# Kernel tuning notes

Hardware: AMD Instinct MI355X
Metric: run time of the kernel (lower is better)

Reference implementation:

```python
import jax, jax.numpy as jnp
import numpy as np

B, T, V, S = 32, 2048, 1024, 256
BLANK = 0
NEG = -1e30  # log-space 'zero' (avoids inf so zero_infinity handling is a simple threshold)


def setup_inputs() -> dict:
    key = jax.random.key(0)
    k1, k2, k3, k4 = jax.random.split(key, 4)
    # valid log-probabilities, as produced by an upstream log_softmax head
    preds_logprob = jax.nn.log_softmax(
        jax.random.normal(k1, (B, T, V), dtype=jnp.float32), axis=-1)
    tokens_gt = jax.random.randint(k2, (B, S), 1, V)            # labels exclude blank=0
    cqt_lens = jax.random.randint(k3, (B,), T // 2, T + 1)      # input lengths
    token_lens_gt = jax.random.randint(k4, (B,), S // 2, S + 1) # target lengths (>=1)
    return {"preds_logprob": preds_logprob, "tokens_gt": tokens_gt,
            "cqt_lens": cqt_lens, "token_lens_gt": token_lens_gt}


def _ctc_single(lp, ext, rep_ok, Tl, Sl):
    """Negative CTC log-likelihood for one sample.
    lp: [T, V] log-probs; ext: [L=2S+1] extended label seq (blanks interleaved);
    rep_ok: [L] bool, whether the s-2 -> s skip transition is allowed;
    Tl: input length; Sl: target length (>=1)."""
    emit = lp[:, ext]  # [T, L] emission log-probs, gathered once outside the scan
    L = ext.shape[0]
    alpha = jnp.full((L,), NEG, dtype=lp.dtype)
    alpha = alpha.at[0].set(emit[0, 0]).at[1].set(emit[0, 1])

    neg1 = jnp.full((1,), NEG, dtype=lp.dtype)
    neg2 = jnp.full((2,), NEG, dtype=lp.dtype)

    def step(alpha, xs):
        e, t = xs
        a1 = jnp.concatenate([neg1, alpha[:-1]])
        a2 = jnp.concatenate([neg2, alpha[:-2]])
        a2 = jnp.where(rep_ok, a2, NEG)
        m = jnp.maximum(jnp.maximum(alpha, a1), a2)
        new = e + m + jnp.log(jnp.exp(alpha - m) + jnp.exp(a1 - m) + jnp.exp(a2 - m))
        # freeze the lattice past this sample's input length (masking by cqt_lens)
        alpha = jnp.where(t < Tl, new, alpha)
        return alpha, None

    ts = jnp.arange(1, lp.shape[0])
    alpha, _ = jax.lax.scan(step, alpha, (emit[1:], ts))

    # log-likelihood = logsumexp over the two terminal lattice states
    lA = alpha[2 * Sl]
    lB = alpha[2 * Sl - 1]
    m = jnp.maximum(lA, lB)
    ll = m + jnp.log(jnp.exp(lA - m) + jnp.exp(lB - m))
    return -ll


def _ctc_loss(preds_logprob, tokens_gt, cqt_lens, token_lens_gt):
    # mask_by_length: zero out frames past cqt_lens (no effect on CTC value,
    # kept for faithfulness); swapaxes(0,1) is a pure layout change.
    tmask = jnp.arange(T)[None, :] < cqt_lens[:, None]          # [B, T]
    lp = preds_logprob * tmask[:, :, None].astype(preds_logprob.dtype)

    # extended label sequence with blanks interleaved: [blank, y1, blank, ..., yS, blank]
    ext = jnp.zeros((B, 2 * S + 1), dtype=tokens_gt.dtype).at[:, 1::2].set(tokens_gt)
    ext_m2 = jnp.concatenate([jnp.zeros((B, 2), dtype=ext.dtype), ext[:, :-2]], axis=1)
    rep_ok = (ext != BLANK) & (ext != ext_m2)                   # allow s-2 skip

    losses = jax.vmap(_ctc_single)(lp, ext, rep_ok, cqt_lens, token_lens_gt)  # [B]
    # zero_infinity=True: unreachable alignments produce ~ -NEG; zero them out
    losses = jnp.where(losses > 1e29, 0.0, losses)
    # reduction='mean': divide by target length, then mean over batch
    return jnp.mean(losses / token_lens_gt.astype(losses.dtype))


def reference(preds_logprob, tokens_gt, cqt_lens, token_lens_gt):
    return _ctc_loss(preds_logprob, tokens_gt, cqt_lens, token_lens_gt)
```

## Files before the change

kernel.cpp:

```cpp
#include <hip/hip_runtime.h>
#include <math.h>

#define BB 32
#define TT 2048
#define VV 1024
#define SS 256
#define TCHUNK 4
#define CH 16
#define NSLOT 3

__device__ __forceinline__ void async_ld16(const float* g, const float* l) {
    __builtin_amdgcn_global_load_lds(
        (const __attribute__((address_space(1))) void*)(uintptr_t)g,
        (__attribute__((address_space(3))) void*)(unsigned)(uintptr_t)l, 16, 0, 0);
}
__device__ __forceinline__ void async_ld4(const float* g, const float* l) {
    __builtin_amdgcn_global_load_lds(
        (const __attribute__((address_space(1))) void*)(uintptr_t)g,
        (__attribute__((address_space(3))) void*)(unsigned)(uintptr_t)l, 4, 0, 0);
}
#define WAIT_VM0() __builtin_amdgcn_s_waitcnt(0x0F70)

__device__ __forceinline__ float dpp_shr1_f(float x) {
    int r = __builtin_amdgcn_update_dpp(0, __float_as_int(x), 0x138, 0xF, 0xF, true);
    return __int_as_float(r);
}
__device__ __forceinline__ int dpp_shr1_i(int x) {
    return __builtin_amdgcn_update_dpp(0, x, 0x138, 0xF, 0xF, true);
}
__device__ __forceinline__ float max3f(float a, float b, float c) {
    float d;
    asm("v_max3_f32 %0, %1, %2, %3" : "=v"(d) : "v"(a), "v"(b), "v"(c));
    return d;
}

__global__ __launch_bounds__(256) void ctc_pre(const float* __restrict__ lp,
    const int* __restrict__ tokens, const int* __restrict__ cqt,
    const int* __restrict__ slen, float* __restrict__ G, float* __restrict__ Gbl,
    float* __restrict__ out)
{
    __shared__ __align__(16) float rows[TCHUNK][VV];
    __shared__ int toks[SS];
    const int tid = threadIdx.x;
    const int bx  = blockIdx.x;
    if (bx == 0 && tid == 0) out[0] = 0.f;
    const int nchunk = TT / TCHUNK;
    const int b  = bx / nchunk;
    const int t0 = (bx % nchunk) * TCHUNK;
    const int Tl = cqt[b];
    if (t0 >= Tl) return;
    const int Sl = slen[b];
    toks[tid] = tokens[b * SS + tid];
#pragma unroll
    for (int k = 0; k < TCHUNK; ++k) {
        const int t = t0 + k;
        if (t < Tl)
            ((float4*)rows[k])[tid] = ((const float4*)(lp + ((size_t)b * TT + t) * VV))[tid];
    }
    __syncthreads();
#pragma unroll
    for (int k = 0; k < TCHUNK; ++k) {
        const int t = t0 + k;
        if (t >= Tl) break;
        const float pb0 = rows[k][0];
        float* gp = G + ((size_t)b * TT + t) * 256;
        gp[tid] = (tid < Sl) ? __expf(rows[k][toks[tid]] - pb0) : 0.f;
        if (tid == 0) Gbl[b * TT + t] = pb0;
    }
}

__global__ __launch_bounds__(256) void ctc_walk(const float* __restrict__ G,
    const float* __restrict__ Gbl, const int* __restrict__ tokens,
    const int* __restrict__ cqt, const int* __restrict__ slen, float* __restrict__ out)
{
    __shared__ __align__(16) float tokL[NSLOT][CH * 256];
    __shared__ __align__(16) float blkL[NSLOT][64];
    __shared__ float als[513];
    __shared__ int   aE[65];
    __shared__ int   ready[NSLOT];
    __shared__ int   prog;

    const int b    = blockIdx.x;
    const int tid  = threadIdx.x;
    const int wid  = tid >> 6;
    const int lane = tid & 63;
    const int Tl   = cqt[b];
    const float* __restrict__ Gb   = G   + (size_t)b * TT * 256;
    const float* __restrict__ GblB = Gbl + (size_t)b * TT;

    if (tid < NSLOT) ready[tid] = -1;
    if (tid == NSLOT) prog = -1;
    __syncthreads();

    const int NC = (Tl + 14) >> 4;
    volatile int* vready = ready;
    volatile int* vprog  = &prog;

    if (wid != 0) {
        const int slot = wid - 1;
        for (int c = wid - 1; c < NC; c += 3) {
            while (*vprog < c - NSLOT) {}
            __builtin_amdgcn_sched_barrier(0);
            asm volatile("" ::: "memory");
            const int tbase = 1 + (c << 4);
            const float* lt = tokL[slot];
#pragma unroll
            for (int k = 0; k < CH; ++k) {
                int tt = tbase + k; tt = (tt < Tl) ? tt : (Tl - 1);
                async_ld16(Gb + (size_t)tt * 256 + (lane << 2), lt + k * 256);
            }
            int tbk = tbase + lane; tbk = (tbk < Tl) ? tbk : (Tl - 1);
            async_ld4(GblB + tbk, blkL[slot]);
            WAIT_VM0();
            __builtin_amdgcn_sched_barrier(0);
            asm volatile("" ::: "memory");
            vready[slot] = c;
        }
        return;
    }

    const int Sl = slen[b];
    const int j0 = lane * 4;
    const int* tb = tokens + b * SS;
    const int tm1 = (j0 == 0) ? 0 : tb[j0 - 1];
    const int q0 = tb[j0], q1 = tb[j0 + 1], q2 = tb[j0 + 2], q3 = tb[j0 + 3];
    const float m0 = (q0 != tm1) ? 1.f : 0.f;
    const float m1 = (q1 != q0)  ? 1.f : 0.f;
    const float m2 = (q2 != q1)  ? 1.f : 0.f;
    const float m3 = (q3 != q2)  ? 1.f : 0.f;
    const float lzm = (lane == 0) ? 0.f : 1.f;

    float a0=0.f,a1=0.f,a2=0.f,a3=0.f,a4=0.f,a5=0.f,a6=0.f,a7=0.f,aX=0.f;
    if (lane == 0) {
        const float e0 = __expf(GblB[0]);
        a0 = e0;
        a1 = Gb[0] * e0;
    }
    int    Etot = 0;
    float  sfac = lzm;
    double bacc = 0.0;

#define LOADCHUNK(s) do { \
    _Pragma("unroll") \
    for (int k = 0; k < CH; ++k) { \
        pr[k] = ((const float4*)(tokL[s] + (k << 8)))[lane]; \
        pb[k] = blkL[s][k]; \
    } \
} while (0)

#define ONESTEP(P4) do { \
    const float h1 = dpp_shr1_f(a7) * sfac; \
    const float n0 = a0 + h1; \
    const float n1 = (P4).x * (a1 + a0 + m0 * h1); \
    const float n2 = a2 + a1; \
    const float n3 = (P4).y * (a3 + a2 + m1 * a1); \
    const float n4 = a4 + a3; \
    const float n5 = (P4).z * (a5 + a4 + m2 * a3); \
    const float n6 = a6 + a5; \
    const float n7 = (P4).w * (a7 + a6 + m3 * a5); \
    aX = aX + a7; \
    a0=n0;a1=n1;a2=n2;a3=n3;a4=n4;a5=n5;a6=n6;a7=n7; \
} while (0)

#define RENORM_LOCAL() do { \
    const float mm = max3f(max3f(a0,a1,a2), max3f(a3,a4,a5), max3f(a6,a7,aX)); \
    int ee = (__float_as_int(mm) >> 23) - 126; \
    ee = (mm > 0.f) ? ee : 0; \
    const float sc = __int_as_float((127 - ee) << 23); \
    a0*=sc;a1*=sc;a2*=sc;a3*=sc;a4*=sc;a5*=sc;a6*=sc;a7*=sc;aX*=sc; \
    Etot += ee; \
    int Ep = dpp_shr1_i(Etot); \
    if (mm == 0.f && lane > 0) Etot = Ep; \
    Ep = dpp_shr1_i(Etot); \
    if (mm == 0.f && lane > 0) Etot = Ep; \
    int dd = Ep - Etot; \
    dd = (dd < -126) ? -126 : ((dd > 100) ? 100 : dd); \
    sfac = __int_as_float((127 + dd) << 23) * lzm; \
} while (0)

    float4 pr[CH];
    float  pb[CH];

    const int F = (Tl - 1) >> 4;
    int slot = 0;
    for (int c = 0; c < NC; ++c) {
        while (vready[slot] < c) {}
        __builtin_amdgcn_sched_barrier(0);
        asm volatile("" ::: "memory");
        LOADCHUNK(slot);
        asm volatile("" ::: "memory");
        *vprog = c;
        if (c < F) {
            float bt = ((pb[0]+pb[1])+(pb[2]+pb[3]))+((pb[4]+pb[5])+(pb[6]+pb[7]));
            bt += ((pb[8]+pb[9])+(pb[10]+pb[11]))+((pb[12]+pb[13])+(pb[14]+pb[15]));
            bacc += (double)bt;
#pragma unroll
            for (int k = 0; k < CH; ++k) {
                ONESTEP(pr[k]);
                if ((k & 3) == 3) RENORM_LOCAL();
            }
        } else {
            const int nv = (Tl - 1) - (F << 4);
            float bt = 0.f;
#pragma unroll
            for (int k = 0; k < CH; ++k) {
                if (k < nv) { bt += pb[k]; ONESTEP(pr[k]); }
                if ((k & 3) == 3) RENORM_LOCAL();
            }
            bacc += (double)bt;
        }
        slot = (slot == NSLOT - 1) ? 0 : slot + 1;
    }

    als[8 * lane + 0] = a0; als[8 * lane + 1] = a1;
    als[8 * lane + 2] = a2; als[8 * lane + 3] = a3;
    als[8 * lane + 4] = a4; als[8 * lane + 5] = a5;
    als[8 * lane + 6] = a6; als[8 * lane + 7] = a7;
    aE[lane] = Etot;
    if (lane == 63) { als[512] = aX; aE[64] = Etot; }
    asm volatile("s_waitcnt lgkmcnt(0)" ::: "memory");
    if (lane == 0) {
        const int sA = 2 * Sl, sB = 2 * Sl - 1;
        const float vA = als[sA], vB = als[sB];
        const int   eA = aE[sA >> 3], eB = aE[sB >> 3];
        int em;
        if (vA > 0.f && vB > 0.f) em = (eA > eB) ? eA : eB;
        else if (vA > 0.f)        em = eA;
        else if (vB > 0.f)        em = eB;
        else                      em = 0;
        const double s = ldexp((double)vA, eA - em) + ldexp((double)vB, eB - em);
        double loss = -(log(s) + (double)em * 0.6931471805599453 + bacc);
        if (!(loss < 1e29)) loss = 0.0;
        atomicAdd(out, (float)(loss / ((double)Sl * (double)BB)));
    }
#undef LOADCHUNK
#undef ONESTEP
#undef RENORM_LOCAL
}

extern "C" void kernel_launch(void* const* d_in, const int* in_sizes, int n_in,
                              void* d_out, int out_size, void* d_ws, size_t ws_size,
                              hipStream_t stream)
{
    const float* lp     = (const float*)d_in[0];
    const int*   tokens = (const int*)d_in[1];
    const int*   cqt    = (const int*)d_in[2];
    const int*   slen   = (const int*)d_in[3];
    float* out = (float*)d_out;
    float* G   = (float*)d_ws;
    float* Gbl = G + (size_t)BB * TT * 256;

    hipLaunchKernelGGL(ctc_pre,  dim3(BB * (TT / TCHUNK)), dim3(256), 0, stream,
                       lp, tokens, cqt, slen, G, Gbl, out);
    hipLaunchKernelGGL(ctc_walk, dim3(BB), dim3(256), 0, stream,
                       G, Gbl, tokens, cqt, slen, out);
}
```

Baseline: 486.0 us.

## Split CTC lattice walk across two wavefronts in a wavefront pipeline

The serial alpha recursion, previously run by a single wavefront owning 8 lattice states per lane, is split so wave 0 handles the first half of the lattice and wave 1 the second half. Each lane now owns 4 states. Wave 0 publishes its boundary value and exponents per chunk through double-buffered shared memory, and wave 1 consumes them one chunk behind. This halves per-step arithmetic on the critical path at the cost of cross-wave spin synchronisation, extra shared-memory traffic and one more wave per block (320 threads).

```diff
diff --git a/kernel.cpp b/kernel.cpp
--- a/kernel.cpp
+++ b/kernel.cpp
@@ -69,16 +69,19 @@
     }
 }
 
-__global__ __launch_bounds__(256) void ctc_walk(const float* __restrict__ G,
+__global__ __launch_bounds__(320) void ctc_walk(const float* __restrict__ G,
     const float* __restrict__ Gbl, const int* __restrict__ tokens,
     const int* __restrict__ cqt, const int* __restrict__ slen, float* __restrict__ out)
 {
     __shared__ __align__(16) float tokL[NSLOT][CH * 256];
     __shared__ __align__(16) float blkL[NSLOT][64];
+    __shared__ float hbuf[2][CH][64];
+    __shared__ int   eabuf[2][4][64];
     __shared__ float als[513];
-    __shared__ int   aE[65];
+    __shared__ int   aE[129];
+    __shared__ double baccS;
     __shared__ int   ready[NSLOT];
-    __shared__ int   prog;
+    __shared__ int   prog, hready, afin;
 
     const int b    = blockIdx.x;
     const int tid  = threadIdx.x;
@@ -89,16 +92,21 @@
     const float* __restrict__ GblB = Gbl + (size_t)b * TT;
 
     if (tid < NSLOT) ready[tid] = -1;
-    if (tid == NSLOT) prog = -1;
+    if (tid == NSLOT)     prog   = -1;
+    if (tid == NSLOT + 1) hready = -1;
+    if (tid == NSLOT + 2) afin   = 0;
     __syncthreads();
 
     const int NC = (Tl + 14) >> 4;
-    volatile int* vready = ready;
-    volatile int* vprog  = &prog;
-
-    if (wid != 0) {
-        const int slot = wid - 1;
-        for (int c = wid - 1; c < NC; c += 3) {
+    const int F  = (Tl - 1) >> 4;
+    volatile int* vready  = ready;
+    volatile int* vprog   = &prog;
+    volatile int* vhready = &hready;
+    volatile int* vafin   = &afin;
+
+    if (wid >= 2) {
+        const int slot = wid - 2;
+        for (int c = slot; c < NC; c += 3) {
             while (*vprog < c - NSLOT) {}
             __builtin_amdgcn_sched_barrier(0);
             asm volatile("" ::: "memory");
@@ -120,54 +128,41 @@
     }
 
     const int Sl = slen[b];
-    const int j0 = lane * 4;
     const int* tb = tokens + b * SS;
-    const int tm1 = (j0 == 0) ? 0 : tb[j0 - 1];
-    const int q0 = tb[j0], q1 = tb[j0 + 1], q2 = tb[j0 + 2], q3 = tb[j0 + 3];
-    const float m0 = (q0 != tm1) ? 1.f : 0.f;
-    const float m1 = (q1 != q0)  ? 1.f : 0.f;
-    const float m2 = (q2 != q1)  ? 1.f : 0.f;
-    const float m3 = (q3 != q2)  ? 1.f : 0.f;
-    const float lzm = (lane == 0) ? 0.f : 1.f;
-
-    float a0=0.f,a1=0.f,a2=0.f,a3=0.f,a4=0.f,a5=0.f,a6=0.f,a7=0.f,aX=0.f;
-    if (lane == 0) {
-        const float e0 = __expf(GblB[0]);
-        a0 = e0;
-        a1 = Gb[0] * e0;
-    }
-    int    Etot = 0;
-    float  sfac = lzm;
-    double bacc = 0.0;
-
-#define LOADCHUNK(s) do { \
-    _Pragma("unroll") \
-    for (int k = 0; k < CH; ++k) { \
-        pr[k] = ((const float4*)(tokL[s] + (k << 8)))[lane]; \
-        pb[k] = blkL[s][k]; \
-    } \
+
+    if (wid == 0) {
+        const int jA  = lane * 2;
+        const int tm1 = (lane == 0) ? 0 : tb[jA - 1];
+        const int q0 = tb[jA], q1 = tb[jA + 1];
+        const float m0 = (q0 != tm1) ? 1.f : 0.f;
+        const float m1 = (q1 != q0)  ? 1.f : 0.f;
+        const float lzm = (lane == 0) ? 0.f : 1.f;
+
+        float a0=0.f,a1=0.f,a2=0.f,a3=0.f;
+        if (lane == 0) {
+            const float e0 = __expf(GblB[0]);
+            a0 = e0;
+            a1 = Gb[0] * e0;
+        }
+        int    Etot = 0;
+        float  sfac = lzm;
+        double bacc = 0.0;
+
+#define ONESTEP_A(P2) do { \
+    const float h1 = dpp_shr1_f(a3) * sfac; \
+    const float n0 = a0 + h1; \
+    const float n1 = (P2).x * (a1 + a0 + m0 * h1); \
+    const float n2 = a2 + a1; \
+    const float n3 = (P2).y * (a3 + a2 + m1 * a1); \
+    a0=n0;a1=n1;a2=n2;a3=n3; \
 } while (0)
 
-#define ONESTEP(P4) do { \
-    const float h1 = dpp_shr1_f(a7) * sfac; \
-    const float n0 = a0 + h1; \
-    const float n1 = (P4).x * (a1 + a0 + m0 * h1); \
-    const float n2 = a2 + a1; \
-    const float n3 = (P4).y * (a3 + a2 + m1 * a1); \
-    const float n4 = a4 + a3; \
-    const float n5 = (P4).z * (a5 + a4 + m2 * a3); \
-    const float n6 = a6 + a5; \
-    const float n7 = (P4).w * (a7 + a6 + m3 * a5); \
-    aX = aX + a7; \
-    a0=n0;a1=n1;a2=n2;a3=n3;a4=n4;a5=n5;a6=n6;a7=n7; \
-} while (0)
-
-#define RENORM_LOCAL() do { \
-    const float mm = max3f(max3f(a0,a1,a2), max3f(a3,a4,a5), max3f(a6,a7,aX)); \
+#define RENORM_A() do { \
+    const float mm = fmaxf(max3f(a0,a1,a2), a3); \
     int ee = (__float_as_int(mm) >> 23) - 126; \
     ee = (mm > 0.f) ? ee : 0; \
     const float sc = __int_as_float((127 - ee) << 23); \
-    a0*=sc;a1*=sc;a2*=sc;a3*=sc;a4*=sc;a5*=sc;a6*=sc;a7*=sc;aX*=sc; \
+    a0*=sc;a1*=sc;a2*=sc;a3*=sc; \
     Etot += ee; \
     int Ep = dpp_shr1_i(Etot); \
     if (mm == 0.f && lane > 0) Etot = Ep; \
@@ -178,64 +173,160 @@
     sfac = __int_as_float((127 + dd) << 23) * lzm; \
 } while (0)
 
-    float4 pr[CH];
-    float  pb[CH];
-
-    const int F = (Tl - 1) >> 4;
-    int slot = 0;
-    for (int c = 0; c < NC; ++c) {
-        while (vready[slot] < c) {}
-        __builtin_amdgcn_sched_barrier(0);
+        float2 pr[CH];
+        float  pb[CH];
+        int slot = 0;
+        for (int c = 0; c < NC; ++c) {
+            while (vready[slot] < c) {}
+            while (*vprog < c - 2) {}
+            __builtin_amdgcn_sched_barrier(0);
+            asm volatile("" ::: "memory");
+#pragma unroll
+            for (int k = 0; k < CH; ++k) {
+                pr[k] = *(const float2*)(tokL[slot] + (k << 8) + (lane << 1));
+                pb[k] = blkL[slot][k];
+            }
+            const int par = c & 1;
+            float* hb = &hbuf[par][0][0];
+            int*   eb = &eabuf[par][0][0];
+            if (c < F) {
+                float bt = ((pb[0]+pb[1])+(pb[2]+pb[3]))+((pb[4]+pb[5])+(pb[6]+pb[7]));
+                bt += ((pb[8]+pb[9])+(pb[10]+pb[11]))+((pb[12]+pb[13])+(pb[14]+pb[15]));
+                bacc += (double)bt;
+#pragma unroll
+                for (int k = 0; k < CH; ++k) {
+                    ONESTEP_A(pr[k]);
+                    if ((k & 3) == 3) { RENORM_A(); eb[((k >> 2) << 6) + lane] = Etot; }
+                    hb[(k << 6) + lane] = a3;
+                }
+            } else {
+                const int nv = (Tl - 1) - (F << 4);
+                float bt = 0.f;
+#pragma unroll
+                for (int k = 0; k < CH; ++k) {
+                    if (k < nv) { bt += pb[k]; ONESTEP_A(pr[k]); }
+                    if ((k & 3) == 3) { RENORM_A(); eb[((k >> 2) << 6) + lane] = Etot; }
+                    hb[(k << 6) + lane] = a3;
+                }
+                bacc += (double)bt;
+            }
+            asm volatile("" ::: "memory");
+            *vhready = c;
+            slot = (slot == NSLOT - 1) ? 0 : slot + 1;
+        }
+        als[4 * lane + 0] = a0; als[4 * lane + 1] = a1;
+        als[4 * lane + 2] = a2; als[4 * lane + 3] = a3;
+        aE[lane] = Etot;
+        if (lane == 0) baccS = bacc;
+        asm volatile("s_waitcnt lgkmcnt(0)" ::: "memory");
+        *vafin = 1;
+        return;
+#undef ONESTEP_A
+#undef RENORM_A
+    }
+
+    {
+        const int jB  = 128 + lane * 2;
+        const int q0 = tb[jB], q1 = tb[jB + 1];
+        const int tm1 = tb[jB - 1];
+        const float m0 = (q0 != tm1) ? 1.f : 0.f;
+        const float m1 = (q1 != q0)  ? 1.f : 0.f;
+
+        float a0=0.f,a1=0.f,a2=0.f,a3=0.f,aX=0.f;
+        int   Etot = 0;
+        float sfac = 1.f;
+        float hprev = 0.f;
+
+#define ONESTEP_B(P2, HIN) do { \
+    float hx = dpp_shr1_f(a3); \
+    hx = (lane == 0) ? (HIN) : hx; \
+    const float h1 = hx * sfac; \
+    const float n0 = a0 + h1; \
+    const float n1 = (P2).x * (a1 + a0 + m0 * h1); \
+    const float n2 = a2 + a1; \
+    const float n3 = (P2).y * (a3 + a2 + m1 * a1); \
+    aX = aX + a3; \
+    a0=n0;a1=n1;a2=n2;a3=n3; \
+} while (0)
+
+#define RENORM_B(g) do { \
+    const float mm = fmaxf(max3f(a0,a1,a2), fmaxf(a3,aX)); \
+    int ee = (__float_as_int(mm) >> 23) - 126; \
+    ee = (mm > 0.f) ? ee : 0; \
+    const float sc = __int_as_float((127 - ee) << 23); \
+    a0*=sc;a1*=sc;a2*=sc;a3*=sc;aX*=sc; \
+    Etot += ee; \
+    int Ep = dpp_shr1_i(Etot); \
+    Ep = (lane == 0) ? ea[g] : Ep; \
+    if (mm == 0.f) Etot = Ep; \
+    Ep = dpp_shr1_i(Etot); \
+    Ep = (lane == 0) ? ea[g] : Ep; \
+    if (mm == 0.f) Etot = Ep; \
+    int dd = Ep - Etot; \
+    dd = (dd < -126) ? -126 : ((dd > 100) ? 100 : dd); \
+    sfac = __int_as_float((127 + dd) << 23); \
+} while (0)
+
+        float2 pr[CH];
+        float  hk[CH];
+        int    ea[4];
+        int slot = 0;
+        for (int c = 0; c < NC; ++c) {
+            while (*vhready < c) {}
+            __builtin_amdgcn_sched_barrier(0);
+            asm volatile("" ::: "memory");
+            const int par = c & 1;
+#pragma unroll
+            for (int k = 0; k < CH; ++k) {
+                pr[k] = *(const float2*)(tokL[slot] + (k << 8) + 128 + (lane << 1));
+                hk[k] = hbuf[par][k][63];
+            }
+#pragma unroll
+            for (int g = 0; g < 4; ++g) ea[g] = eabuf[par][g][63];
+            asm volatile("" ::: "memory");
+            *vprog = c;
+            if (c < F) {
+#pragma unroll
+                for (int k = 0; k < CH; ++k) {
+                    ONESTEP_B(pr[k], (k == 0) ? hprev : hk[k - 1]);
+                    if ((k & 3) == 3) RENORM_B(k >> 2);
+                }
+                hprev = hk[CH - 1];
+            } else {
+                const int nv = (Tl - 1) - (F << 4);
+#pragma unroll
+                for (int k = 0; k < CH; ++k) {
+                    if (k < nv) ONESTEP_B(pr[k], (k == 0) ? hprev : hk[k - 1]);
+                    if ((k & 3) == 3) RENORM_B(k >> 2);
+                }
+            }
+            slot = (slot == NSLOT - 1) ? 0 : slot + 1;
+        }
+
+        als[256 + 4 * lane + 0] = a0; als[256 + 4 * lane + 1] = a1;
+        als[256 + 4 * lane + 2] = a2; als[256 + 4 * lane + 3] = a3;
+        aE[64 + lane] = Etot;
+        if (lane == 63) { als[512] = aX; aE[128] = Etot; }
+        asm volatile("s_waitcnt lgkmcnt(0)" ::: "memory");
+        while (*vafin == 0) {}
         asm volatile("" ::: "memory");
-        LOADCHUNK(slot);
-        asm volatile("" ::: "memory");
-        *vprog = c;
-        if (c < F) {
-            float bt = ((pb[0]+pb[1])+(pb[2]+pb[3]))+((pb[4]+pb[5])+(pb[6]+pb[7]));
-            bt += ((pb[8]+pb[9])+(pb[10]+pb[11]))+((pb[12]+pb[13])+(pb[14]+pb[15]));
-            bacc += (double)bt;
-#pragma unroll
-            for (int k = 0; k < CH; ++k) {
-                ONESTEP(pr[k]);
-                if ((k & 3) == 3) RENORM_LOCAL();
-            }
-        } else {
-            const int nv = (Tl - 1) - (F << 4);
-            float bt = 0.f;
-#pragma unroll
-            for (int k = 0; k < CH; ++k) {
-                if (k < nv) { bt += pb[k]; ONESTEP(pr[k]); }
-                if ((k & 3) == 3) RENORM_LOCAL();
-            }
-            bacc += (double)bt;
-        }
-        slot = (slot == NSLOT - 1) ? 0 : slot + 1;
-    }
-
-    als[8 * lane + 0] = a0; als[8 * lane + 1] = a1;
-    als[8 * lane + 2] = a2; als[8 * lane + 3] = a3;
-    als[8 * lane + 4] = a4; als[8 * lane + 5] = a5;
-    als[8 * lane + 6] = a6; als[8 * lane + 7] = a7;
-    aE[lane] = Etot;
-    if (lane == 63) { als[512] = aX; aE[64] = Etot; }
-    asm volatile("s_waitcnt lgkmcnt(0)" ::: "memory");
-    if (lane == 0) {
-        const int sA = 2 * Sl, sB = 2 * Sl - 1;
-        const float vA = als[sA], vB = als[sB];
-        const int   eA = aE[sA >> 3], eB = aE[sB >> 3];
-        int em;
-        if (vA > 0.f && vB > 0.f) em = (eA > eB) ? eA : eB;
-        else if (vA > 0.f)        em = eA;
-        else if (vB > 0.f)        em = eB;
-        else                      em = 0;
-        const double s = ldexp((double)vA, eA - em) + ldexp((double)vB, eB - em);
-        double loss = -(log(s) + (double)em * 0.6931471805599453 + bacc);
-        if (!(loss < 1e29)) loss = 0.0;
-        atomicAdd(out, (float)(loss / ((double)Sl * (double)BB)));
-    }
-#undef LOADCHUNK
-#undef ONESTEP
-#undef RENORM_LOCAL
+        if (lane == 0) {
+            const int sA = 2 * Sl, sB = 2 * Sl - 1;
+            const float vA = als[sA], vB = als[sB];
+            const int   eA = aE[sA >> 2], eB = aE[sB >> 2];
+            int em;
+            if (vA > 0.f && vB > 0.f) em = (eA > eB) ? eA : eB;
+            else if (vA > 0.f)        em = eA;
+            else if (vB > 0.f)        em = eB;
+            else                      em = 0;
+            const double s = ldexp((double)vA, eA - em) + ldexp((double)vB, eB - em);
+            double loss = -(log(s) + (double)em * 0.6931471805599453 + baccS);
+            if (!(loss < 1e29)) loss = 0.0;
+            atomicAdd(out, (float)(loss / ((double)Sl * (double)BB)));
+        }
+#undef ONESTEP_B
+#undef RENORM_B
+    }
 }
 
 extern "C" void kernel_launch(void* const* d_in, const int* in_sizes, int n_in,
@@ -252,6 +343,6 @@
 
     hipLaunchKernelGGL(ctc_pre,  dim3(BB * (TT / TCHUNK)), dim3(256), 0, stream,
                        lp, tokens, cqt, slen, G, Gbl, out);
-    hipLaunchKernelGGL(ctc_walk, dim3(BB), dim3(256), 0, stream,
+    hipLaunchKernelGGL(ctc_walk, dim3(BB), dim3(320), 0, stream,
                        G, Gbl, tokens, cqt, slen, out);
 }
```

Result: faster. 466.7 us (-4.0%).
